# Optimization experiments

Hardware: AMD Instinct MI355X
Metric: run time of the kernel (lower is better)

The kernel has to match this reference:

```python
import jax, jax.numpy as jnp
import numpy as np

C = 256
C4 = C // 4  # 64
B = 4
N = 4096
FACTOR = float(np.sqrt(C4))


def setup_inputs() -> dict:
    key = jax.random.key(0)
    k1, k2, k3, k4 = jax.random.split(key, 4)
    x = jax.random.normal(k1, (B, C, N), dtype=jnp.float32)
    # q_conv and k_conv share the SAME weight (tied in the torch module)
    W_qk = jax.random.normal(k2, (C4, C), dtype=jnp.float32) * (1.0 / np.sqrt(C))
    W_v = jax.random.normal(k3, (C4, C), dtype=jnp.float32) * (1.0 / np.sqrt(C))
    b_v = jax.random.normal(k4, (C4,), dtype=jnp.float32) * 0.01
    return {"x": x, "W_qk": W_qk, "W_v": W_v, "b_v": b_v}


def reference(x, W_qk, W_v, b_v):
    # Conv1d with kernel size 1 == per-position linear: [B,C,N] -> [B,C4,N]
    x_q = jnp.einsum('oc,bcn->bon', W_qk, x)          # [B, C4, N]
    x_k = x_q                                          # tied weights: k == q
    x_v = jnp.einsum('oc,bcn->bon', W_v, x) + b_v[None, :, None]  # [B, C4, N]
    # energy = x_k.permute(0,2,1) @ x_q : [B, N, N]
    energy = jnp.einsum('bcn,bcm->bnm', x_k, x_q) / FACTOR
    attention = jax.nn.softmax(energy, axis=-1)        # softmax over last dim
    x_r = jnp.einsum('bcn,bnm->bcm', x_v, attention)   # [B, C4, N]
    return x_r
```

## Files before the change

### kernel.cpp

```cpp
#include <hip/hip_runtime.h>


#define CC 256
#define C4C 64
#define NBATCH 4
#define NN 4096
#define QSCALE 0.42466089f
#define SHIFT2 12.0f

typedef _Float16 f16;
typedef _Float16 half2v __attribute__((ext_vector_type(2)));
typedef _Float16 half4 __attribute__((ext_vector_type(4)));
typedef _Float16 half8 __attribute__((ext_vector_type(8)));
typedef __fp16 fp16x2 __attribute__((ext_vector_type(2)));
typedef float floatx4 __attribute__((ext_vector_type(4)));

static __device__ __forceinline__ half2v pkrtz(float a, float b) {
  fp16x2 r = __builtin_amdgcn_cvt_pkrtz(a, b);
  return __builtin_bit_cast(half2v, r);
}

#define LOADQ(T, A0, A1)                                                   \
  { const f16* p_ = Qb + (size_t)(T) * 1024 + l * 8;                       \
    A0 = *(const half8*)(p_); A1 = *(const half8*)(p_ + 512); }

#define XT_PITCH 264
__global__ __launch_bounds__(256) void qv_kernel(
    const float* __restrict__ x, const float* __restrict__ Wqk,
    const float* __restrict__ Wv, const float* __restrict__ bv,
    f16* __restrict__ Qtb, f16* __restrict__ V4)
{
  __shared__ __align__(16) f16 xt[32][XT_PITCH];
  const int b = blockIdx.y;
  const int n0 = blockIdx.x * 32;
  const int tid = threadIdx.x;

  {
    const int nq = tid & 7;
    const int cb = tid >> 3;
    const int c = cb * 8;
    const float* xp = x + (size_t)b * CC * NN + n0 + nq * 4;
    float4 r[8];
#pragma unroll
    for (int j = 0; j < 8; ++j)
      r[j] = *(const float4*)(xp + (size_t)(c + j) * NN);
#pragma unroll
    for (int s = 0; s < 4; ++s) {
      half8 h;
#pragma unroll
      for (int j = 0; j < 8; ++j) h[j] = (f16)(((const float*)&r[j])[s]);
      *(half8*)(&xt[nq * 4 + s][c]) = h;
    }
  }

  const int w = tid >> 6, l = tid & 63, lr = l & 15, lg = l >> 4;
  const float* Wsrc = (w < 2) ? Wqk : Wv;
  const int ocb = (w & 1) * 32;
  half8 af[2][8];
#pragma unroll
  for (int t = 0; t < 2; ++t) {
    const float* wp = Wsrc + (size_t)(ocb + t * 16 + lr) * CC + 8 * lg;
#pragma unroll
    for (int kk = 0; kk < 8; ++kk) {
      float4 wa = *(const float4*)(wp + kk * 32);
      float4 wb = *(const float4*)(wp + kk * 32 + 4);
      half8 h;
      h[0] = (f16)wa.x; h[1] = (f16)wa.y; h[2] = (f16)wa.z; h[3] = (f16)wa.w;
      h[4] = (f16)wb.x; h[5] = (f16)wb.y; h[6] = (f16)wb.z; h[7] = (f16)wb.w;
      af[t][kk] = h;
    }
  }

  __syncthreads();

  floatx4 acc[2][2] = {{{0.f,0.f,0.f,0.f},{0.f,0.f,0.f,0.f}},
                       {{0.f,0.f,0.f,0.f},{0.f,0.f,0.f,0.f}}};
#pragma unroll
  for (int nt = 0; nt < 2; ++nt) {
#pragma unroll
    for (int kk = 0; kk < 8; ++kk) {
      half8 bf = *(const half8*)(&xt[nt * 16 + lr][kk * 32 + 8 * lg]);
      acc[0][nt] = __builtin_amdgcn_mfma_f32_16x16x32_f16(af[0][kk], bf, acc[0][nt], 0, 0, 0);
      acc[1][nt] = __builtin_amdgcn_mfma_f32_16x16x32_f16(af[1][kk], bf, acc[1][nt], 0, 0, 0);
    }
  }

  if (w < 2) {
#pragma unroll
    for (int t = 0; t < 2; ++t)
#pragma unroll
      for (int nt = 0; nt < 2; ++nt) {
        int T = (n0 >> 4) + nt;
        int kg = 2 * t + (lg >> 1);
        union { f16 h[4]; unsigned long long u; } q4;
#pragma unroll
        for (int i = 0; i < 4; ++i) q4.h[i] = (f16)(acc[t][nt][i] * QSCALE);
        *(unsigned long long*)(Qtb + (size_t)(b * 256 + T) * 1024 + w * 512
                               + (kg * 16 + lr) * 8 + (lg & 1) * 4) = q4.u;
      }
  } else {
#pragma unroll
    for (int t = 0; t < 2; ++t)
#pragma unroll
      for (int nt = 0; nt < 2; ++nt) {
        int T = (n0 >> 4) + nt;
        int oc = (w - 2) * 32 + t * 16 + 4 * lg;
#pragma unroll
        for (int i = 0; i < 4; ++i)
          V4[(size_t)(b * 256 + T) * 1024 + (oc + i) * 16 + lr] =
              (f16)(acc[t][nt][i] + bv[oc + i]);
      }
  }
}

#define Z_PRELOAD(TBEG)                                                    \
  { _Pragma("unroll")                                                      \
    for (int mt = 0; mt < 8; ++mt) {                                       \
      const f16* p_ = Qb + (size_t)((TBEG) + mt) * 1024 + l * 8;           \
      bb[mt][0] = *(const half8*)(p_);                                     \
      bb[mt][1] = *(const half8*)(p_ + 512);                               \
    } }

#define Z_E(MT, D0, D1)                                                    \
  { D0 = (floatx4){0.f,0.f,0.f,0.f}; D1 = (floatx4){0.f,0.f,0.f,0.f};      \
    D0 = __builtin_amdgcn_mfma_f32_16x16x32_f16(a[0][0], bb[MT][0], D0, 0, 0, 0); \
    D1 = __builtin_amdgcn_mfma_f32_16x16x32_f16(a[1][0], bb[MT][0], D1, 0, 0, 0); \
    D0 = __builtin_amdgcn_mfma_f32_16x16x32_f16(a[0][1], bb[MT][1], D0, 0, 0, 0); \
    D1 = __builtin_amdgcn_mfma_f32_16x16x32_f16(a[1][1], bb[MT][1], D1, 0, 0, 0); }

#define Z_SM(D0, D1)                                                       \
  { _Pragma("unroll")                                                      \
    for (int i = 0; i < 4; ++i) {                                          \
      rs[0][i] += __builtin_amdgcn_exp2f(D0[i]);                           \
      rs[1][i] += __builtin_amdgcn_exp2f(D1[i]); } }

#define Z_TILES17                                                          \
  Z_E(1, dB0, dB1); Z_SM(dA0, dA1);                                        \
  Z_E(2, dA0, dA1); Z_SM(dB0, dB1);                                        \
  Z_E(3, dB0, dB1); Z_SM(dA0, dA1);                                        \
  Z_E(4, dA0, dA1); Z_SM(dB0, dB1);                                        \
  Z_E(5, dB0, dB1); Z_SM(dA0, dA1);                                        \
  Z_E(6, dA0, dA1); Z_SM(dB0, dB1);                                        \
  Z_E(7, dB0, dB1); Z_SM(dA0, dA1);

__global__ __launch_bounds__(256) void z_kernel(
    const f16* __restrict__ Qtb, float* __restrict__ Zinv)
{
  __shared__ float zl[4][32];
  const int bx = blockIdx.x;
  const int xcd = bx & 7, slot = bx >> 3;
  const int b = xcd >> 1;
  const int wu = ((xcd & 1) << 6) | slot;
  const int n0 = wu * 32;
  const int tid = threadIdx.x;
  const int w = tid >> 6, l = tid & 63, lr = l & 15, lg = l >> 4;
  const f16* Qb = Qtb + (size_t)b * 256 * 1024;

  half8 a[2][2];
  LOADQ((n0 >> 4), a[0][0], a[0][1]);
  LOADQ((n0 >> 4) + 1, a[1][0], a[1][1]);

  const int tstr = w * 64;
  half8 bb[8][2];
  floatx4 dA0, dA1, dB0, dB1;
  float rs[2][4] = {{0.f,0.f,0.f,0.f},{0.f,0.f,0.f,0.f}};

  Z_PRELOAD(tstr);
  Z_E(0, dA0, dA1);
  Z_TILES17;
#pragma unroll 1
  for (int mch = 1; mch < 8; ++mch) {
    Z_PRELOAD(tstr + mch * 8);
    Z_SM(dB0, dB1);
    Z_E(0, dA0, dA1);
    Z_TILES17;
  }
  Z_SM(dB0, dB1);

#pragma unroll
  for (int t = 0; t < 2; ++t)
#pragma unroll
    for (int i = 0; i < 4; ++i) {
      float v = rs[t][i];
      v += __shfl_xor(v, 1); v += __shfl_xor(v, 2);
      v += __shfl_xor(v, 4); v += __shfl_xor(v, 8);
      rs[t][i] = v;
    }
  if (lr == 0) {
#pragma unroll
    for (int t = 0; t < 2; ++t)
#pragma unroll
      for (int i = 0; i < 4; ++i)
        zl[w][16 * t + 4 * lg + i] = rs[t][i];
  }
  __syncthreads();
  if (tid < 32) {
    float s = zl[0][tid] + zl[1][tid] + zl[2][tid] + zl[3][tid];
    Zinv[b * NN + n0 + tid] = 4096.0f / s;
  }
}

#define LOADV(NB, UA)                                                      \
  { const f16* up_ = Vb + (size_t)(NB) * 1024 + 4 * lg;                    \
    _Pragma("unroll")                                                      \
    for (int cs = 0; cs < 4; ++cs)                                         \
      UA[cs] = *(const half4*)(up_ + (16 * cs + lr) * 16); }

__global__ __launch_bounds__(512, 4) void av_kernel(
    const f16* __restrict__ Qtb, const f16* __restrict__ V4,
    const float* __restrict__ Zinv, float* __restrict__ Out)
{
  __shared__ float red[8][2][16][17];

  const int bx = blockIdx.x;
  const int xcd = bx & 7, slot = bx >> 3;
  const int b = xcd >> 1;
  const int m0 = (((xcd & 1) << 6) | slot) * 32;
  const int tid = threadIdx.x;
  const int w = tid >> 6;
  const int l = tid & 63;
  const int lr = l & 15, lg = l >> 4;

  const f16* Qb = Qtb + (size_t)b * 256 * 1024;
  const f16* Vb = V4 + (size_t)b * 256 * 1024;
  const float* Zb = Zinv + b * NN;

  half8 bq[2][2];
  LOADQ((m0 >> 4), bq[0][0], bq[0][1]);
  LOADQ((m0 >> 4) + 1, bq[1][0], bq[1][1]);

  floatx4 o[4][2];
#pragma unroll
  for (int cs = 0; cs < 4; ++cs)
#pragma unroll
    for (int t = 0; t < 2; ++t) o[cs][t] = (floatx4){0.f, 0.f, 0.f, 0.f};

#pragma unroll 2
  for (int it = 0; it < 32; ++it) {
    const int T = it * 8 + w;
    half8 a0, a1;
    LOADQ(T, a0, a1);
    half4 va[4];
    LOADV(T, va);
    const float4 zi = *(const float4*)(Zb + T * 16 + 4 * lg);

    floatx4 dA = {-SHIFT2, -SHIFT2, -SHIFT2, -SHIFT2};
    floatx4 dB = {-SHIFT2, -SHIFT2, -SHIFT2, -SHIFT2};
    dA = __builtin_amdgcn_mfma_f32_16x16x32_f16(a0, bq[0][0], dA, 0, 0, 0);
    dB = __builtin_amdgcn_mfma_f32_16x16x32_f16(a0, bq[1][0], dB, 0, 0, 0);
    dA = __builtin_amdgcn_mfma_f32_16x16x32_f16(a1, bq[0][1], dA, 0, 0, 0);
    dB = __builtin_amdgcn_mfma_f32_16x16x32_f16(a1, bq[1][1], dB, 0, 0, 0);

    half2v p0a = pkrtz(__builtin_amdgcn_exp2f(dA[0]) * zi.x,
                       __builtin_amdgcn_exp2f(dA[1]) * zi.y);
    half2v p0b = pkrtz(__builtin_amdgcn_exp2f(dA[2]) * zi.z,
                       __builtin_amdgcn_exp2f(dA[3]) * zi.w);
    half2v p1a = pkrtz(__builtin_amdgcn_exp2f(dB[0]) * zi.x,
                       __builtin_amdgcn_exp2f(dB[1]) * zi.y);
    half2v p1b = pkrtz(__builtin_amdgcn_exp2f(dB[2]) * zi.z,
                       __builtin_amdgcn_exp2f(dB[3]) * zi.w);
    half4 bt0 = {p0a[0], p0a[1], p0b[0], p0b[1]};
    half4 bt1 = {p1a[0], p1a[1], p1b[0], p1b[1]};
#pragma unroll
    for (int cs = 0; cs < 4; ++cs) {
      o[cs][0] = __builtin_amdgcn_mfma_f32_16x16x16f16(va[cs], bt0, o[cs][0], 0, 0, 0);
      o[cs][1] = __builtin_amdgcn_mfma_f32_16x16x16f16(va[cs], bt1, o[cs][1], 0, 0, 0);
    }
  }

#pragma unroll 1
  for (int cs = 0; cs < 4; ++cs) {
    __syncthreads();
#pragma unroll
    for (int t = 0; t < 2; ++t)
#pragma unroll
      for (int i = 0; i < 4; ++i)
        red[w][t][4 * lg + i][lr] = o[cs][t][i];
    __syncthreads();
    const int t = tid >> 8;
    const int r = (tid >> 4) & 15;
    const int col = tid & 15;
    float ssum = 0.f;
#pragma unroll
    for (int ww = 0; ww < 8; ++ww) ssum += red[ww][t][r][col];
    Out[((size_t)b * C4C + cs * 16 + r) * NN + m0 + t * 16 + col] = ssum;
  }
}

extern "C" void kernel_launch(void* const* d_in, const int* in_sizes, int n_in,
                              void* d_out, int out_size, void* d_ws, size_t ws_size,
                              hipStream_t stream)
{
  const float* x   = (const float*)d_in[0];
  const float* Wqk = (const float*)d_in[1];
  const float* Wv  = (const float*)d_in[2];
  const float* bv  = (const float*)d_in[3];
  float* out = (float*)d_out;

  char* ws = (char*)d_ws;
  f16*   Qtb  = (f16*)(ws);
  f16*   V4   = (f16*)(ws + (2u << 20));
  float* Zinv = (float*)(ws + (4u << 20));

  qv_kernel<<<dim3(128, 4), 256, 0, stream>>>(x, Wqk, Wv, bv, Qtb, V4);
  z_kernel<<<dim3(512), 256, 0, stream>>>(Qtb, Zinv);
  av_kernel<<<dim3(512), 512, 0, stream>>>(Qtb, V4, Zinv, out);
}
```

Measured before the change: 61.21 us.

## Retile softmax-denominator kernel to 64 rows per block with 8 waves

The z_kernel now gives each block 64 query rows instead of 32 and runs 8 waves instead of 4. Each wave sweeps 32 key tiles across four chunks, and every loaded K tile is reused against four A tiles instead of two. This halves the grid and the redundant global loads of K per query row. It drops the explicit software pipelining that interleaved MFMA with exp2 across register sets, leaving scheduling to the compiler, and it uses more registers per wave.

```diff
diff --git a/kernel.cpp b/kernel.cpp
--- a/kernel.cpp
+++ b/kernel.cpp
@@ -113,72 +113,58 @@
   }
 }
 
-#define Z_PRELOAD(TBEG)                                                    \
-  { _Pragma("unroll")                                                      \
-    for (int mt = 0; mt < 8; ++mt) {                                       \
-      const f16* p_ = Qb + (size_t)((TBEG) + mt) * 1024 + l * 8;           \
-      bb[mt][0] = *(const half8*)(p_);                                     \
-      bb[mt][1] = *(const half8*)(p_ + 512);                               \
-    } }
-
-#define Z_E(MT, D0, D1)                                                    \
-  { D0 = (floatx4){0.f,0.f,0.f,0.f}; D1 = (floatx4){0.f,0.f,0.f,0.f};      \
-    D0 = __builtin_amdgcn_mfma_f32_16x16x32_f16(a[0][0], bb[MT][0], D0, 0, 0, 0); \
-    D1 = __builtin_amdgcn_mfma_f32_16x16x32_f16(a[1][0], bb[MT][0], D1, 0, 0, 0); \
-    D0 = __builtin_amdgcn_mfma_f32_16x16x32_f16(a[0][1], bb[MT][1], D0, 0, 0, 0); \
-    D1 = __builtin_amdgcn_mfma_f32_16x16x32_f16(a[1][1], bb[MT][1], D1, 0, 0, 0); }
-
-#define Z_SM(D0, D1)                                                       \
-  { _Pragma("unroll")                                                      \
-    for (int i = 0; i < 4; ++i) {                                          \
-      rs[0][i] += __builtin_amdgcn_exp2f(D0[i]);                           \
-      rs[1][i] += __builtin_amdgcn_exp2f(D1[i]); } }
-
-#define Z_TILES17                                                          \
-  Z_E(1, dB0, dB1); Z_SM(dA0, dA1);                                        \
-  Z_E(2, dA0, dA1); Z_SM(dB0, dB1);                                        \
-  Z_E(3, dB0, dB1); Z_SM(dA0, dA1);                                        \
-  Z_E(4, dA0, dA1); Z_SM(dB0, dB1);                                        \
-  Z_E(5, dB0, dB1); Z_SM(dA0, dA1);                                        \
-  Z_E(6, dA0, dA1); Z_SM(dB0, dB1);                                        \
-  Z_E(7, dB0, dB1); Z_SM(dA0, dA1);
-
-__global__ __launch_bounds__(256) void z_kernel(
+__global__ __launch_bounds__(512) void z_kernel(
     const f16* __restrict__ Qtb, float* __restrict__ Zinv)
 {
-  __shared__ float zl[4][32];
+  __shared__ float zl[8][64];
   const int bx = blockIdx.x;
   const int xcd = bx & 7, slot = bx >> 3;
   const int b = xcd >> 1;
-  const int wu = ((xcd & 1) << 6) | slot;
-  const int n0 = wu * 32;
+  const int wu = ((xcd & 1) << 5) | slot;
+  const int n0t = wu * 4;
   const int tid = threadIdx.x;
   const int w = tid >> 6, l = tid & 63, lr = l & 15, lg = l >> 4;
   const f16* Qb = Qtb + (size_t)b * 256 * 1024;
 
-  half8 a[2][2];
-  LOADQ((n0 >> 4), a[0][0], a[0][1]);
-  LOADQ((n0 >> 4) + 1, a[1][0], a[1][1]);
-
-  const int tstr = w * 64;
-  half8 bb[8][2];
-  floatx4 dA0, dA1, dB0, dB1;
-  float rs[2][4] = {{0.f,0.f,0.f,0.f},{0.f,0.f,0.f,0.f}};
-
-  Z_PRELOAD(tstr);
-  Z_E(0, dA0, dA1);
-  Z_TILES17;
+  half8 a[4][2];
+#pragma unroll
+  for (int t = 0; t < 4; ++t) LOADQ(n0t + t, a[t][0], a[t][1]);
+
+  const int tstr = w * 32;
+  float rs[4][4];
+#pragma unroll
+  for (int t = 0; t < 4; ++t)
+#pragma unroll
+    for (int i = 0; i < 4; ++i) rs[t][i] = 0.f;
+
 #pragma unroll 1
-  for (int mch = 1; mch < 8; ++mch) {
-    Z_PRELOAD(tstr + mch * 8);
-    Z_SM(dB0, dB1);
-    Z_E(0, dA0, dA1);
-    Z_TILES17;
-  }
-  Z_SM(dB0, dB1);
-
-#pragma unroll
-  for (int t = 0; t < 2; ++t)
+  for (int ch = 0; ch < 4; ++ch) {
+    half8 bb[8][2];
+#pragma unroll
+    for (int mt = 0; mt < 8; ++mt) {
+      const f16* p_ = Qb + (size_t)(tstr + ch * 8 + mt) * 1024 + l * 8;
+      bb[mt][0] = *(const half8*)(p_);
+      bb[mt][1] = *(const half8*)(p_ + 512);
+    }
+#pragma unroll
+    for (int mt = 0; mt < 8; ++mt) {
+      floatx4 d[4];
+#pragma unroll
+      for (int t = 0; t < 4; ++t) {
+        d[t] = (floatx4){0.f, 0.f, 0.f, 0.f};
+        d[t] = __builtin_amdgcn_mfma_f32_16x16x32_f16(a[t][0], bb[mt][0], d[t], 0, 0, 0);
+        d[t] = __builtin_amdgcn_mfma_f32_16x16x32_f16(a[t][1], bb[mt][1], d[t], 0, 0, 0);
+      }
+#pragma unroll
+      for (int t = 0; t < 4; ++t)
+#pragma unroll
+        for (int i = 0; i < 4; ++i)
+          rs[t][i] += __builtin_amdgcn_exp2f(d[t][i]);
+    }
+  }
+
+#pragma unroll
+  for (int t = 0; t < 4; ++t)
 #pragma unroll
     for (int i = 0; i < 4; ++i) {
       float v = rs[t][i];
@@ -188,15 +174,17 @@
     }
   if (lr == 0) {
 #pragma unroll
-    for (int t = 0; t < 2; ++t)
+    for (int t = 0; t < 4; ++t)
 #pragma unroll
       for (int i = 0; i < 4; ++i)
         zl[w][16 * t + 4 * lg + i] = rs[t][i];
   }
   __syncthreads();
-  if (tid < 32) {
-    float s = zl[0][tid] + zl[1][tid] + zl[2][tid] + zl[3][tid];
-    Zinv[b * NN + n0 + tid] = 4096.0f / s;
+  if (tid < 64) {
+    float s = 0.f;
+#pragma unroll
+    for (int ww = 0; ww < 8; ++ww) s += zl[ww][tid];
+    Zinv[b * NN + n0t * 16 + tid] = 4096.0f / s;
   }
 }
 
@@ -303,6 +291,6 @@
   float* Zinv = (float*)(ws + (4u << 20));
 
   qv_kernel<<<dim3(128, 4), 256, 0, stream>>>(x, Wqk, Wv, bv, Qtb, V4);
-  z_kernel<<<dim3(512), 256, 0, stream>>>(Qtb, Zinv);
+  z_kernel<<<dim3(256), 512, 0, stream>>>(Qtb, Zinv);
   av_kernel<<<dim3(512), 512, 0, stream>>>(Qtb, V4, Zinv, out);
 }
```

New measurement: 60.50 us (median of 2 runs). Within noise of the previous version (-1.2%).
